# Performance work log

Hardware: AMD Instinct MI355X
Metric: run time of the kernel (lower is better)

Reference implementation:

```python
import jax, jax.numpy as jnp
import numpy as np

M = 8192      # nodes
D = 128       # feature dim
DEG = 32      # neighbors per node


def setup_inputs() -> dict:
    key = jax.random.key(0)
    ks = jax.random.split(key, 6)
    z = jax.random.normal(ks[0], (M, D), dtype=jnp.float32)
    # deterministic, duplicate-free edge list: node i -> (i+1..i+DEG) mod M
    src = jnp.repeat(jnp.arange(M, dtype=jnp.int64), DEG)
    dst = (src + jnp.tile(jnp.arange(1, DEG + 1, dtype=jnp.int64), M)) % M
    edge_index = jnp.stack([src, dst], axis=0)  # [2, M*DEG]
    s = 1.0 / np.sqrt(D)
    Wg = jax.random.normal(ks[1], (D, D), dtype=jnp.float32) * s
    Wc = jax.random.normal(ks[2], (D, D), dtype=jnp.float32) * s
    Wq = jax.random.normal(ks[3], (D, D), dtype=jnp.float32) * s
    Wk = jax.random.normal(ks[4], (D, D), dtype=jnp.float32) * s
    a = jax.random.normal(ks[5], (2 * D,), dtype=jnp.float32)
    return {"z": z, "edge_index": edge_index, "Wg": Wg, "Wc": Wc,
            "Wq": Wq, "Wk": Wk, "a": a}


def reference(z, edge_index, Wg, Wc, Wq, Wk, a):
    m, d = z.shape
    wg = z @ Wg.T                              # [m, d]
    src, dst = edge_index[0], edge_index[1]
    a_src, a_dst = a[:d], a[d:]
    # per-edge score: leaky_relu(a . [wg[i], wg[j]]) = leaky_relu(a1.wg[i] + a2.wg[j])
    scores = jax.nn.leaky_relu((wg @ a_src)[src] + (wg @ a_dst)[dst])  # [E]
    # softmax over each source node's neighbors (segment softmax)
    smax = jax.ops.segment_max(scores, src, num_segments=m)
    ex = jnp.exp(scores - smax[src])
    denom = jax.ops.segment_sum(ex, src, num_segments=m)
    alpha = ex / denom[src]                    # [E]
    # scatter-aggregate: local[i] = sum_j alpha_ij * wg[j]
    local = jax.ops.segment_sum(alpha[:, None] * wg[dst], src, num_segments=m)
    # dense global attention branch
    q = z @ Wq.T
    k = z @ Wk.T
    beta = jax.nn.softmax(q @ k.T / jnp.sqrt(jnp.float32(d)), axis=-1)  # [m, m]
    global_msg = beta @ (z @ Wc.T)
    return jax.nn.leaky_relu(local + global_msg + z)
```

## Files before the change

### kernel.cpp

```cpp
#include <hip/hip_runtime.h>

#define MM 8192
#define DD 128
#define DEG 32
#define KSPLIT 16
#define BK 32
#define NTILE 16
#define NB 16
#define RSTAGE 48

typedef __attribute__((ext_vector_type(8))) _Float16 h8;
typedef __attribute__((ext_vector_type(4))) float f4;
typedef __attribute__((ext_vector_type(4))) unsigned int u4;
typedef __attribute__((ext_vector_type(4))) short s4;

__device__ __forceinline__ unsigned short f2h(float f) {
  _Float16 h = (_Float16)f;
  return __builtin_bit_cast(unsigned short, h);
}

__device__ __forceinline__ void lds_dma16(const unsigned short* gptr, unsigned short* lptr) {
  __builtin_amdgcn_global_load_lds(
      (const __attribute__((address_space(1))) unsigned int*)gptr,
      (__attribute__((address_space(3))) unsigned int*)lptr, 16, 0, 0);
}

__global__ __launch_bounds__(256) void proj_kernel(
    const float* __restrict__ z, const float* __restrict__ Wg,
    const float* __restrict__ Wc, const float* __restrict__ Wq,
    const float* __restrict__ Wk, const float* __restrict__ a,
    float* __restrict__ wg, unsigned short* __restrict__ qb,
    unsigned short* __restrict__ kb, unsigned short* __restrict__ ct,
    float* __restrict__ sg, float* __restrict__ sd)
{
  __shared__ unsigned short zt[64 * 136];
  __shared__ unsigned short wt[128 * 136];
  const int mode = blockIdx.y;
  const float* __restrict__ W = (mode == 0) ? Wg : (mode == 1) ? Wq : (mode == 2) ? Wk : Wc;
  const int r0 = blockIdx.x * 64;
  const int tid = threadIdx.x;

  #pragma unroll
  for (int it = 0; it < 8; ++it) {
    int id = tid + it * 256, row = id >> 5, c4 = (id & 31) * 4;
    f4 v = *(const f4*)(z + (r0 + row) * DD + c4);
    s4 sv = {(short)f2h(v.x), (short)f2h(v.y), (short)f2h(v.z), (short)f2h(v.w)};
    *(s4*)&zt[row * 136 + c4] = sv;
  }
  #pragma unroll
  for (int it = 0; it < 16; ++it) {
    int id = tid + it * 256, row = id >> 5, c4 = (id & 31) * 4;
    f4 v = *(const f4*)(W + row * DD + c4);
    s4 sv = {(short)f2h(v.x), (short)f2h(v.y), (short)f2h(v.z), (short)f2h(v.w)};
    *(s4*)&wt[row * 136 + c4] = sv;
  }
  __syncthreads();

  const int lane = tid & 63, w = tid >> 6, n = lane & 15, quad = lane >> 4;
  h8 afr[4];
  #pragma unroll
  for (int kt = 0; kt < 4; ++kt)
    afr[kt] = *(const h8*)&zt[(16 * w + n) * 136 + kt * 32 + quad * 8];

  f4 acc[8];
  const f4 fzero = {0.f, 0.f, 0.f, 0.f};
  #pragma unroll
  for (int nt = 0; nt < 8; ++nt) {
    f4 c = fzero;
    #pragma unroll
    for (int kt = 0; kt < 4; ++kt) {
      h8 b = *(const h8*)&wt[(16 * nt + n) * 136 + kt * 32 + quad * 8];
      c = __builtin_amdgcn_mfma_f32_16x16x32_f16(afr[kt], b, c, 0, 0, 0);
    }
    acc[nt] = c;
  }

  if (mode == 0) {
    #pragma unroll
    for (int nt = 0; nt < 8; ++nt)
      #pragma unroll
      for (int r = 0; r < 4; ++r)
        wg[(r0 + 16 * w + quad * 4 + r) * DD + 16 * nt + n] = acc[nt][r];
    float av[8], bv[8];
    #pragma unroll
    for (int nt = 0; nt < 8; ++nt) { av[nt] = a[16 * nt + n]; bv[nt] = a[DD + 16 * nt + n]; }
    #pragma unroll
    for (int r = 0; r < 4; ++r) {
      float s1 = 0.f, s2 = 0.f;
      #pragma unroll
      for (int nt = 0; nt < 8; ++nt) { s1 += acc[nt][r] * av[nt]; s2 += acc[nt][r] * bv[nt]; }
      s1 += __shfl_xor(s1, 1); s1 += __shfl_xor(s1, 2); s1 += __shfl_xor(s1, 4); s1 += __shfl_xor(s1, 8);
      s2 += __shfl_xor(s2, 1); s2 += __shfl_xor(s2, 2); s2 += __shfl_xor(s2, 4); s2 += __shfl_xor(s2, 8);
      if (n == 0) {
        int g = r0 + 16 * w + quad * 4 + r;
        sg[g] = s1; sd[g] = s2;
      }
    }
  } else if (mode == 1) {
    const float qscale = 0.12752551286084110f;
    #pragma unroll
    for (int nt = 0; nt < 8; ++nt)
      #pragma unroll
      for (int r = 0; r < 4; ++r)
        qb[(r0 + 16 * w + quad * 4 + r) * DD + 16 * nt + n] = f2h(acc[nt][r] * qscale);
  } else if (mode == 2) {
    #pragma unroll
    for (int nt = 0; nt < 8; ++nt)
      #pragma unroll
      for (int r = 0; r < 4; ++r)
        kb[(r0 + 16 * w + quad * 4 + r) * DD + 16 * nt + n] = f2h(acc[nt][r]);
  } else {
    __syncthreads();
    #pragma unroll
    for (int nt = 0; nt < 8; ++nt)
      #pragma unroll
      for (int r = 0; r < 4; ++r)
        wt[(16 * nt + n) * 80 + 16 * w + quad * 4 + r] = f2h(acc[nt][r]);
    __syncthreads();
    #pragma unroll
    for (int it = 0; it < 4; ++it) {
      int idx = tid + it * 256, d = idx >> 3, c8 = (idx & 7) * 8;
      u4 v = *(const u4*)&wt[d * 80 + c8];
      *(u4*)(ct + (size_t)d * MM + r0 + c8) = v;
    }
  }
}

__global__ __launch_bounds__(256, 2) void flash_kernel(
    const unsigned short* __restrict__ qb, const unsigned short* __restrict__ kb,
    const unsigned short* __restrict__ ct, unsigned short* __restrict__ Opart,
    float* __restrict__ Lpart)
{
  __shared__ unsigned short sh[18944];
  const int bid = blockIdx.x + (blockIdx.y << 6);
  const int ck = bid & 15, qt = bid >> 4;
  const int tid = threadIdx.x, lane = tid & 63, w = tid >> 6;
  const int n = lane & 15, quad = lane >> 4;
  const int ln = n, lq = quad;
  const int qr0 = qt * 128;

  #pragma unroll
  for (int it = 0; it < 8; ++it)
    lds_dma16(qb + (qr0 + it * 16 + ln) * DD + w * 32 + lq * 8,
              &sh[(it * 256 + tid) * 8]);
  __syncthreads();
  h8 aq[2][4];
  #pragma unroll
  for (int mt = 0; mt < 2; ++mt)
    #pragma unroll
    for (int kt = 0; kt < 4; ++kt)
      aq[mt][kt] = *(const h8*)&sh[((w * 2 + mt) * 4 + kt) * 512 + lane * 8];
  __syncthreads();

  const unsigned short* kp = kb + (size_t)(ck * 512 + 2 * ln) * DD + w * 32 + lq * 8;
  const unsigned short* vp = ct + (size_t)(16 * w + ln) * MM + ck * 512 + lq * 8;

  #pragma unroll
  for (int it = 0; it < 2; ++it)
    lds_dma16(kp + it * DD, &sh[(it * 256 + tid) * 8]);
  #pragma unroll
  for (int it = 0; it < 2; ++it)
    lds_dma16(vp + (size_t)it * 64 * MM, &sh[4096 + (it * 256 + tid) * 8]);

  f4 acc_o[2][8];
  const f4 fzero = {0.f, 0.f, 0.f, 0.f};
  #pragma unroll
  for (int mt = 0; mt < 2; ++mt)
    #pragma unroll
    for (int dt = 0; dt < 8; ++dt) acc_o[mt][dt] = fzero;
  float l_r[2][4] = {{0.f, 0.f, 0.f, 0.f}, {0.f, 0.f, 0.f, 0.f}};
  const int pbase = 16384 + w * 640;

  for (int t = 0; t < NTILE; ++t) {
    __syncthreads();
    const int cur = (t & 1) * 8192;

    if (t < NTILE - 1) {
      const int nb = ((t + 1) & 1) * 8192;
      const unsigned short* kpn = kp + (size_t)(t + 1) * BK * DD;
      const unsigned short* vpn = vp + (t + 1) * BK;
      #pragma unroll
      for (int it = 0; it < 2; ++it)
        lds_dma16(kpn + it * DD, &sh[nb + (it * 256 + tid) * 8]);
      #pragma unroll
      for (int it = 0; it < 2; ++it)
        lds_dma16(vpn + (size_t)it * 64 * MM, &sh[nb + 4096 + (it * 256 + tid) * 8]);
    }

    f4 accs[2][2];
    accs[0][0] = fzero; accs[0][1] = fzero; accs[1][0] = fzero; accs[1][1] = fzero;
    __builtin_amdgcn_s_setprio(1);
    #pragma unroll
    for (int nt = 0; nt < 2; ++nt) {
      #pragma unroll
      for (int kt = 0; kt < 4; ++kt) {
        h8 bk = *(const h8*)&sh[cur + nt * 2048 + kt * 512 + lane * 8];
        accs[0][nt] = __builtin_amdgcn_mfma_f32_16x16x32_f16(aq[0][kt], bk, accs[0][nt], 0, 0, 0);
        accs[1][nt] = __builtin_amdgcn_mfma_f32_16x16x32_f16(aq[1][kt], bk, accs[1][nt], 0, 0, 0);
      }
    }
    __builtin_amdgcn_s_setprio(0);

    h8 ap[2];
    #pragma unroll
    for (int mt = 0; mt < 2; ++mt) {
      #pragma unroll
      for (int r = 0; r < 4; ++r) {
        float p0 = exp2f(fminf(accs[mt][0][r], 14.4269504f));
        float p1 = exp2f(fminf(accs[mt][1][r], 14.4269504f));
        l_r[mt][r] += p0 + p1;
        auto pv = __builtin_amdgcn_cvt_pkrtz(p0, p1);
        *(unsigned int*)&sh[pbase + (quad * 4 + r) * 40 + 2 * n] =
            __builtin_bit_cast(unsigned int, pv);
      }
      ap[mt] = *(const h8*)&sh[pbase + n * 40 + quad * 8];
    }

    __builtin_amdgcn_s_setprio(1);
    #pragma unroll
    for (int dt = 0; dt < 8; ++dt) {
      h8 bv = *(const h8*)&sh[cur + 4096 + dt * 512 + lane * 8];
      acc_o[0][dt] = __builtin_amdgcn_mfma_f32_16x16x32_f16(ap[0], bv, acc_o[0][dt], 0, 0, 0);
      acc_o[1][dt] = __builtin_amdgcn_mfma_f32_16x16x32_f16(ap[1], bv, acc_o[1][dt], 0, 0, 0);
    }
    __builtin_amdgcn_s_setprio(0);
  }

  #pragma unroll
  for (int mt = 0; mt < 2; ++mt)
    #pragma unroll
    for (int r = 0; r < 4; ++r) {
      float lv = l_r[mt][r];
      lv += __shfl_xor(lv, 1); lv += __shfl_xor(lv, 2);
      lv += __shfl_xor(lv, 4); lv += __shfl_xor(lv, 8);
      int g = qr0 + w * 32 + mt * 16 + quad * 4 + r;
      if (n == 0) Lpart[ck * MM + g] = lv;
      #pragma unroll
      for (int dt = 0; dt < 8; ++dt)
        Opart[((size_t)ck * MM + g) * DD + 16 * dt + n] = f2h(acc_o[mt][dt][r]);
    }
}

__global__ __launch_bounds__(256) void merge_kernel(
    const int* __restrict__ ei, const float* __restrict__ wg,
    const float* __restrict__ sg, const float* __restrict__ sd,
    const unsigned short* __restrict__ Opart, const float* __restrict__ Lpart,
    const float* __restrict__ z, float* __restrict__ out)
{
  __shared__ float rows_s[RSTAGE * 132];
  __shared__ float sc_s[NB][DEG];
  __shared__ float alpha_s[NB][DEG];
  __shared__ int idx_s[NB][DEG];
  const int tid = threadIdx.x;
  const int i0 = blockIdx.x * NB;

  #pragma unroll
  for (int it = 0; it < 6; ++it) {
    int idx = tid + it * 256;
    int r = idx >> 5, c4 = (idx & 31) * 4;
    int grow = (i0 + 1 + r) & (MM - 1);
    *(f4*)&rows_s[r * 132 + c4] = *(const f4*)(wg + (size_t)grow * DD + c4);
  }
  #pragma unroll
  for (int it = 0; it < 2; ++it) {
    int e = tid + it * 256;
    int nj = e >> 5, j = e & 31;
    int i = i0 + nj;
    int dstj = ei[MM * DEG + i * DEG + j];
    float s = sg[i] + sd[dstj];
    sc_s[nj][j] = s > 0.f ? s : 0.01f * s;
    idx_s[nj][j] = (dstj - (i0 + 1)) & (MM - 1);
  }
  __syncthreads();

  const int ni = tid >> 4, l16 = tid & 15;
  {
    float s0 = sc_s[ni][l16], s1 = sc_s[ni][l16 + 16];
    float mx = fmaxf(s0, s1);
    mx = fmaxf(mx, __shfl_xor(mx, 1)); mx = fmaxf(mx, __shfl_xor(mx, 2));
    mx = fmaxf(mx, __shfl_xor(mx, 4)); mx = fmaxf(mx, __shfl_xor(mx, 8));
    float p0 = __expf(s0 - mx), p1 = __expf(s1 - mx);
    float sum = p0 + p1;
    sum += __shfl_xor(sum, 1); sum += __shfl_xor(sum, 2);
    sum += __shfl_xor(sum, 4); sum += __shfl_xor(sum, 8);
    float inv = 1.f / sum;
    alpha_s[ni][l16] = p0 * inv;
    alpha_s[ni][l16 + 16] = p1 * inv;
  }

  const int d0 = l16 * 8;
  const int i = i0 + ni;
  float acc[8] = {0.f, 0.f, 0.f, 0.f, 0.f, 0.f, 0.f, 0.f};
  #pragma unroll 4
  for (int j = 0; j < DEG; ++j) {
    float al = alpha_s[ni][j];
    int r = idx_s[ni][j];
    if (r < RSTAGE) {
      const float* src = &rows_s[r * 132 + d0];
      #pragma unroll
      for (int q = 0; q < 8; ++q) acc[q] += al * src[q];
    } else {
      const float* src = wg + (size_t)((i0 + 1 + r) & (MM - 1)) * DD + d0;
      #pragma unroll
      for (int q = 0; q < 8; ++q) acc[q] += al * src[q];
    }
  }

  float l = 0.f;
  float o[8] = {0.f, 0.f, 0.f, 0.f, 0.f, 0.f, 0.f, 0.f};
  #pragma unroll
  for (int ck = 0; ck < KSPLIT; ++ck) {
    l += Lpart[ck * MM + i];
    h8 v = *(const h8*)(Opart + ((size_t)ck * MM + i) * DD + d0);
    #pragma unroll
    for (int q = 0; q < 8; ++q) o[q] += (float)v[q];
  }
  float inv = 1.0f / l;
  const float* zp = z + (size_t)i * DD + d0;
  float* op = out + (size_t)i * DD + d0;
  #pragma unroll
  for (int q = 0; q < 8; ++q) {
    float r = o[q] * inv + acc[q] + zp[q];
    op[q] = r > 0.f ? r : 0.01f * r;
  }
}

extern "C" void kernel_launch(void* const* d_in, const int* in_sizes, int n_in,
                              void* d_out, int out_size, void* d_ws, size_t ws_size,
                              hipStream_t stream) {
  const float* z  = (const float*)d_in[0];
  const int*   ei = (const int*)d_in[1];
  const float* Wg = (const float*)d_in[2];
  const float* Wc = (const float*)d_in[3];
  const float* Wq = (const float*)d_in[4];
  const float* Wk = (const float*)d_in[5];
  const float* a  = (const float*)d_in[6];
  float* out = (float*)d_out;
  char* ws = (char*)d_ws;

  float*          wg    = (float*)(ws + 0);
  unsigned short* qb    = (unsigned short*)(ws + (4 << 20));
  unsigned short* kb    = (unsigned short*)(ws + (6 << 20));
  unsigned short* ct    = (unsigned short*)(ws + (8 << 20));
  float*          sg    = (float*)(ws + (10 << 20));
  float*          sd    = (float*)(ws + (10 << 20) + (64 << 10));
  unsigned short* Opart = (unsigned short*)(ws + (11 << 20));
  float*          Lpart = (float*)(ws + (43 << 20));

  proj_kernel<<<dim3(128, 4), 256, 0, stream>>>(z, Wg, Wc, Wq, Wk, a, wg, qb, kb, ct, sg, sd);
  flash_kernel<<<dim3(64, KSPLIT), 256, 0, stream>>>(qb, kb, ct, Opart, Lpart);
  merge_kernel<<<512, 256, 0, stream>>>(ei, wg, sg, sd, Opart, Lpart, z, out);
}
```

Baseline: 133.9 us.

## Software-pipeline flash loop: overlap QK of tile t with PV of tile t-1

```diff
diff --git a/kernel.cpp b/kernel.cpp
--- a/kernel.cpp
+++ b/kernel.cpp
@@ -136,12 +136,11 @@
   const int ck = bid & 15, qt = bid >> 4;
   const int tid = threadIdx.x, lane = tid & 63, w = tid >> 6;
   const int n = lane & 15, quad = lane >> 4;
-  const int ln = n, lq = quad;
   const int qr0 = qt * 128;
 
   #pragma unroll
   for (int it = 0; it < 8; ++it)
-    lds_dma16(qb + (qr0 + it * 16 + ln) * DD + w * 32 + lq * 8,
+    lds_dma16(qb + (qr0 + it * 16 + n) * DD + w * 32 + quad * 8,
               &sh[(it * 256 + tid) * 8]);
   __syncthreads();
   h8 aq[2][4];
@@ -152,17 +151,16 @@
       aq[mt][kt] = *(const h8*)&sh[((w * 2 + mt) * 4 + kt) * 512 + lane * 8];
   __syncthreads();
 
-  const unsigned short* kp = kb + (size_t)(ck * 512 + 2 * ln) * DD + w * 32 + lq * 8;
-  const unsigned short* vp = ct + (size_t)(16 * w + ln) * MM + ck * 512 + lq * 8;
+  const unsigned short* kp = kb + (size_t)(ck * 512 + 2 * n) * DD + w * 32 + quad * 8;
+  const unsigned short* vp = ct + (size_t)(16 * w + n) * MM + ck * 512 + quad * 8;
 
   #pragma unroll
   for (int it = 0; it < 2; ++it)
     lds_dma16(kp + it * DD, &sh[(it * 256 + tid) * 8]);
-  #pragma unroll
-  for (int it = 0; it < 2; ++it)
-    lds_dma16(vp + (size_t)it * 64 * MM, &sh[4096 + (it * 256 + tid) * 8]);
 
   f4 acc_o[2][8];
+  f4 accs[2][2];
+  h8 ap[2];
   const f4 fzero = {0.f, 0.f, 0.f, 0.f};
   #pragma unroll
   for (int mt = 0; mt < 2; ++mt)
@@ -171,60 +169,82 @@
   float l_r[2][4] = {{0.f, 0.f, 0.f, 0.f}, {0.f, 0.f, 0.f, 0.f}};
   const int pbase = 16384 + w * 640;
 
-  for (int t = 0; t < NTILE; ++t) {
+#define QK_TILE(CUR)                                                          \
+  { accs[0][0] = fzero; accs[0][1] = fzero;                                   \
+    accs[1][0] = fzero; accs[1][1] = fzero;                                   \
+    __builtin_amdgcn_s_setprio(1);                                            \
+    _Pragma("unroll")                                                         \
+    for (int nt = 0; nt < 2; ++nt) {                                          \
+      _Pragma("unroll")                                                       \
+      for (int kt = 0; kt < 4; ++kt) {                                        \
+        h8 bk = *(const h8*)&sh[(CUR) + nt * 2048 + kt * 512 + lane * 8];     \
+        accs[0][nt] = __builtin_amdgcn_mfma_f32_16x16x32_f16(aq[0][kt], bk, accs[0][nt], 0, 0, 0); \
+        accs[1][nt] = __builtin_amdgcn_mfma_f32_16x16x32_f16(aq[1][kt], bk, accs[1][nt], 0, 0, 0); \
+      }                                                                       \
+    }                                                                         \
+    __builtin_amdgcn_s_setprio(0); }
+
+#define PV_TILE(PRV)                                                          \
+  { __builtin_amdgcn_s_setprio(1);                                            \
+    _Pragma("unroll")                                                         \
+    for (int dt = 0; dt < 8; ++dt) {                                          \
+      h8 bv = *(const h8*)&sh[(PRV) + 4096 + dt * 512 + lane * 8];            \
+      acc_o[0][dt] = __builtin_amdgcn_mfma_f32_16x16x32_f16(ap[0], bv, acc_o[0][dt], 0, 0, 0); \
+      acc_o[1][dt] = __builtin_amdgcn_mfma_f32_16x16x32_f16(ap[1], bv, acc_o[1][dt], 0, 0, 0); \
+    }                                                                         \
+    __builtin_amdgcn_s_setprio(0); }
+
+#define SOFTMAX_TILE                                                          \
+  { _Pragma("unroll")                                                         \
+    for (int mt = 0; mt < 2; ++mt) {                                          \
+      _Pragma("unroll")                                                       \
+      for (int r = 0; r < 4; ++r) {                                           \
+        float p0 = exp2f(fminf(accs[mt][0][r], 14.4269504f));                 \
+        float p1 = exp2f(fminf(accs[mt][1][r], 14.4269504f));                 \
+        l_r[mt][r] += p0 + p1;                                                \
+        auto pv2 = __builtin_amdgcn_cvt_pkrtz(p0, p1);      \
+        *(unsigned int*)&sh[pbase + (quad * 4 + r) * 40 + 2 * n] =            \
+            __builtin_bit_cast(unsigned int, pv2);                            \
+      }                                                                       \
+      ap[mt] = *(const h8*)&sh[pbase + n * 40 + quad * 8];                    \
+    }                                                                         \
+  }
+
+  __syncthreads();
+  #pragma unroll
+  for (int it = 0; it < 2; ++it)
+    lds_dma16(kp + BK * DD + it * DD, &sh[8192 + (it * 256 + tid) * 8]);
+  #pragma unroll
+  for (int it = 0; it < 2; ++it)
+    lds_dma16(vp + (size_t)it * 64 * MM, &sh[4096 + (it * 256 + tid) * 8]);
+  QK_TILE(0)
+  SOFTMAX_TILE
+
+  for (int t = 1; t < NTILE; ++t) {
     __syncthreads();
     const int cur = (t & 1) * 8192;
+    const int prv = cur ^ 8192;
 
     if (t < NTILE - 1) {
-      const int nb = ((t + 1) & 1) * 8192;
       const unsigned short* kpn = kp + (size_t)(t + 1) * BK * DD;
-      const unsigned short* vpn = vp + (t + 1) * BK;
       #pragma unroll
       for (int it = 0; it < 2; ++it)
-        lds_dma16(kpn + it * DD, &sh[nb + (it * 256 + tid) * 8]);
+        lds_dma16(kpn + it * DD, &sh[prv + (it * 256 + tid) * 8]);
+    }
+    {
+      const unsigned short* vpn = vp + t * BK;
       #pragma unroll
       for (int it = 0; it < 2; ++it)
-        lds_dma16(vpn + (size_t)it * 64 * MM, &sh[nb + 4096 + (it * 256 + tid) * 8]);
-    }
-
-    f4 accs[2][2];
-    accs[0][0] = fzero; accs[0][1] = fzero; accs[1][0] = fzero; accs[1][1] = fzero;
-    __builtin_amdgcn_s_setprio(1);
-    #pragma unroll
-    for (int nt = 0; nt < 2; ++nt) {
-      #pragma unroll
-      for (int kt = 0; kt < 4; ++kt) {
-        h8 bk = *(const h8*)&sh[cur + nt * 2048 + kt * 512 + lane * 8];
-        accs[0][nt] = __builtin_amdgcn_mfma_f32_16x16x32_f16(aq[0][kt], bk, accs[0][nt], 0, 0, 0);
-        accs[1][nt] = __builtin_amdgcn_mfma_f32_16x16x32_f16(aq[1][kt], bk, accs[1][nt], 0, 0, 0);
-      }
-    }
-    __builtin_amdgcn_s_setprio(0);
-
-    h8 ap[2];
-    #pragma unroll
-    for (int mt = 0; mt < 2; ++mt) {
-      #pragma unroll
-      for (int r = 0; r < 4; ++r) {
-        float p0 = exp2f(fminf(accs[mt][0][r], 14.4269504f));
-        float p1 = exp2f(fminf(accs[mt][1][r], 14.4269504f));
-        l_r[mt][r] += p0 + p1;
-        auto pv = __builtin_amdgcn_cvt_pkrtz(p0, p1);
-        *(unsigned int*)&sh[pbase + (quad * 4 + r) * 40 + 2 * n] =
-            __builtin_bit_cast(unsigned int, pv);
-      }
-      ap[mt] = *(const h8*)&sh[pbase + n * 40 + quad * 8];
-    }
-
-    __builtin_amdgcn_s_setprio(1);
-    #pragma unroll
-    for (int dt = 0; dt < 8; ++dt) {
-      h8 bv = *(const h8*)&sh[cur + 4096 + dt * 512 + lane * 8];
-      acc_o[0][dt] = __builtin_amdgcn_mfma_f32_16x16x32_f16(ap[0], bv, acc_o[0][dt], 0, 0, 0);
-      acc_o[1][dt] = __builtin_amdgcn_mfma_f32_16x16x32_f16(ap[1], bv, acc_o[1][dt], 0, 0, 0);
-    }
-    __builtin_amdgcn_s_setprio(0);
-  }
+        lds_dma16(vpn + (size_t)it * 64 * MM, &sh[cur + 4096 + (it * 256 + tid) * 8]);
+    }
+
+    QK_TILE(cur)
+    PV_TILE(prv)
+    SOFTMAX_TILE
+  }
+
+  __syncthreads();
+  PV_TILE(8192)
 
   #pragma unroll
   for (int mt = 0; mt < 2; ++mt)
@@ -239,6 +259,9 @@
       for (int dt = 0; dt < 8; ++dt)
         Opart[((size_t)ck * MM + g) * DD + 16 * dt + n] = f2h(acc_o[mt][dt][r]);
     }
+#undef QK_TILE
+#undef PV_TILE
+#undef SOFTMAX_TILE
 }
 
 __global__ __launch_bounds__(256) void merge_kernel(
```

Result: no change. 133.7 us (-0.1%).

## Halve flash KV splits, double key tile width, add nontemporal partial stores

Applied to the files above, without the earlier changes.

```diff
diff --git a/kernel.cpp b/kernel.cpp
--- a/kernel.cpp
+++ b/kernel.cpp
@@ -3,8 +3,8 @@
 #define MM 8192
 #define DD 128
 #define DEG 32
-#define KSPLIT 16
-#define BK 32
+#define KSPLIT 8
+#define BK 64
 #define NTILE 16
 #define NB 16
 #define RSTAGE 48
@@ -131,17 +131,16 @@
     const unsigned short* __restrict__ ct, unsigned short* __restrict__ Opart,
     float* __restrict__ Lpart)
 {
-  __shared__ unsigned short sh[18944];
+  __shared__ unsigned short sh[37376];
   const int bid = blockIdx.x + (blockIdx.y << 6);
-  const int ck = bid & 15, qt = bid >> 4;
+  const int ck = bid & 7, qt = bid >> 3;
   const int tid = threadIdx.x, lane = tid & 63, w = tid >> 6;
   const int n = lane & 15, quad = lane >> 4;
-  const int ln = n, lq = quad;
   const int qr0 = qt * 128;
 
   #pragma unroll
   for (int it = 0; it < 8; ++it)
-    lds_dma16(qb + (qr0 + it * 16 + ln) * DD + w * 32 + lq * 8,
+    lds_dma16(qb + (qr0 + it * 16 + n) * DD + w * 32 + quad * 8,
               &sh[(it * 256 + tid) * 8]);
   __syncthreads();
   h8 aq[2][4];
@@ -152,15 +151,15 @@
       aq[mt][kt] = *(const h8*)&sh[((w * 2 + mt) * 4 + kt) * 512 + lane * 8];
   __syncthreads();
 
-  const unsigned short* kp = kb + (size_t)(ck * 512 + 2 * ln) * DD + w * 32 + lq * 8;
-  const unsigned short* vp = ct + (size_t)(16 * w + ln) * MM + ck * 512 + lq * 8;
-
-  #pragma unroll
-  for (int it = 0; it < 2; ++it)
+  const unsigned short* kp = kb + (size_t)(ck * 1024 + 4 * n) * DD + w * 32 + quad * 8;
+  const unsigned short* vp = ct + (size_t)(16 * (w >> 1) + n) * MM + ck * 1024 + (w & 1) * 32 + quad * 8;
+
+  #pragma unroll
+  for (int it = 0; it < 4; ++it)
     lds_dma16(kp + it * DD, &sh[(it * 256 + tid) * 8]);
   #pragma unroll
-  for (int it = 0; it < 2; ++it)
-    lds_dma16(vp + (size_t)it * 64 * MM, &sh[4096 + (it * 256 + tid) * 8]);
+  for (int it = 0; it < 4; ++it)
+    lds_dma16(vp + (size_t)it * 32 * MM, &sh[8192 + (it * 256 + tid) * 8]);
 
   f4 acc_o[2][8];
   const f4 fzero = {0.f, 0.f, 0.f, 0.f};
@@ -169,29 +168,31 @@
     #pragma unroll
     for (int dt = 0; dt < 8; ++dt) acc_o[mt][dt] = fzero;
   float l_r[2][4] = {{0.f, 0.f, 0.f, 0.f}, {0.f, 0.f, 0.f, 0.f}};
-  const int pbase = 16384 + w * 640;
+  const int pbase = 32768 + w * 1152;
 
   for (int t = 0; t < NTILE; ++t) {
     __syncthreads();
-    const int cur = (t & 1) * 8192;
+    const int cur = (t & 1) * 16384;
 
     if (t < NTILE - 1) {
-      const int nb = ((t + 1) & 1) * 8192;
+      const int nb = ((t + 1) & 1) * 16384;
       const unsigned short* kpn = kp + (size_t)(t + 1) * BK * DD;
       const unsigned short* vpn = vp + (t + 1) * BK;
       #pragma unroll
-      for (int it = 0; it < 2; ++it)
+      for (int it = 0; it < 4; ++it)
         lds_dma16(kpn + it * DD, &sh[nb + (it * 256 + tid) * 8]);
       #pragma unroll
-      for (int it = 0; it < 2; ++it)
-        lds_dma16(vpn + (size_t)it * 64 * MM, &sh[nb + 4096 + (it * 256 + tid) * 8]);
-    }
-
-    f4 accs[2][2];
-    accs[0][0] = fzero; accs[0][1] = fzero; accs[1][0] = fzero; accs[1][1] = fzero;
-    __builtin_amdgcn_s_setprio(1);
-    #pragma unroll
-    for (int nt = 0; nt < 2; ++nt) {
+      for (int it = 0; it < 4; ++it)
+        lds_dma16(vpn + (size_t)it * 32 * MM, &sh[nb + 8192 + (it * 256 + tid) * 8]);
+    }
+
+    f4 accs[2][4];
+    #pragma unroll
+    for (int mt = 0; mt < 2; ++mt)
+      #pragma unroll
+      for (int nt = 0; nt < 4; ++nt) accs[mt][nt] = fzero;
+    #pragma unroll
+    for (int nt = 0; nt < 4; ++nt) {
       #pragma unroll
       for (int kt = 0; kt < 4; ++kt) {
         h8 bk = *(const h8*)&sh[cur + nt * 2048 + kt * 512 + lane * 8];
@@ -199,31 +200,36 @@
         accs[1][nt] = __builtin_amdgcn_mfma_f32_16x16x32_f16(aq[1][kt], bk, accs[1][nt], 0, 0, 0);
       }
     }
-    __builtin_amdgcn_s_setprio(0);
-
-    h8 ap[2];
+
+    h8 ap[2][2];
     #pragma unroll
     for (int mt = 0; mt < 2; ++mt) {
       #pragma unroll
       for (int r = 0; r < 4; ++r) {
         float p0 = exp2f(fminf(accs[mt][0][r], 14.4269504f));
         float p1 = exp2f(fminf(accs[mt][1][r], 14.4269504f));
-        l_r[mt][r] += p0 + p1;
-        auto pv = __builtin_amdgcn_cvt_pkrtz(p0, p1);
-        *(unsigned int*)&sh[pbase + (quad * 4 + r) * 40 + 2 * n] =
-            __builtin_bit_cast(unsigned int, pv);
+        float p2 = exp2f(fminf(accs[mt][2][r], 14.4269504f));
+        float p3 = exp2f(fminf(accs[mt][3][r], 14.4269504f));
+        l_r[mt][r] += (p0 + p1) + (p2 + p3);
+        auto pk0 = __builtin_amdgcn_cvt_pkrtz(p0, p1);
+        auto pk1 = __builtin_amdgcn_cvt_pkrtz(p2, p3);
+        uint2 pv2; pv2.x = __builtin_bit_cast(unsigned int, pk0);
+        pv2.y = __builtin_bit_cast(unsigned int, pk1);
+        *(uint2*)&sh[pbase + (quad * 4 + r) * 72 + n * 4] = pv2;
       }
-      ap[mt] = *(const h8*)&sh[pbase + n * 40 + quad * 8];
-    }
-
-    __builtin_amdgcn_s_setprio(1);
+      ap[mt][0] = *(const h8*)&sh[pbase + n * 72 + quad * 8];
+      ap[mt][1] = *(const h8*)&sh[pbase + n * 72 + 32 + quad * 8];
+    }
+
     #pragma unroll
     for (int dt = 0; dt < 8; ++dt) {
-      h8 bv = *(const h8*)&sh[cur + 4096 + dt * 512 + lane * 8];
-      acc_o[0][dt] = __builtin_amdgcn_mfma_f32_16x16x32_f16(ap[0], bv, acc_o[0][dt], 0, 0, 0);
-      acc_o[1][dt] = __builtin_amdgcn_mfma_f32_16x16x32_f16(ap[1], bv, acc_o[1][dt], 0, 0, 0);
-    }
-    __builtin_amdgcn_s_setprio(0);
+      #pragma unroll
+      for (int k2 = 0; k2 < 2; ++k2) {
+        h8 bv = *(const h8*)&sh[cur + 8192 + dt * 1024 + k2 * 512 + lane * 8];
+        acc_o[0][dt] = __builtin_amdgcn_mfma_f32_16x16x32_f16(ap[0][k2], bv, acc_o[0][dt], 0, 0, 0);
+        acc_o[1][dt] = __builtin_amdgcn_mfma_f32_16x16x32_f16(ap[1][k2], bv, acc_o[1][dt], 0, 0, 0);
+      }
+    }
   }
 
   #pragma unroll
@@ -234,10 +240,11 @@
       lv += __shfl_xor(lv, 1); lv += __shfl_xor(lv, 2);
       lv += __shfl_xor(lv, 4); lv += __shfl_xor(lv, 8);
       int g = qr0 + w * 32 + mt * 16 + quad * 4 + r;
-      if (n == 0) Lpart[ck * MM + g] = lv;
+      if (n == 0) __builtin_nontemporal_store(lv, &Lpart[ck * MM + g]);
       #pragma unroll
       for (int dt = 0; dt < 8; ++dt)
-        Opart[((size_t)ck * MM + g) * DD + 16 * dt + n] = f2h(acc_o[mt][dt][r]);
+        __builtin_nontemporal_store(f2h(acc_o[mt][dt][r]),
+                                    &Opart[((size_t)ck * MM + g) * DD + 16 * dt + n]);
     }
 }
 
@@ -310,8 +317,8 @@
   float o[8] = {0.f, 0.f, 0.f, 0.f, 0.f, 0.f, 0.f, 0.f};
   #pragma unroll
   for (int ck = 0; ck < KSPLIT; ++ck) {
-    l += Lpart[ck * MM + i];
-    h8 v = *(const h8*)(Opart + ((size_t)ck * MM + i) * DD + d0);
+    l += __builtin_nontemporal_load(&Lpart[ck * MM + i]);
+    h8 v = __builtin_nontemporal_load((const h8*)(Opart + ((size_t)ck * MM + i) * DD + d0));
     #pragma unroll
     for (int q = 0; q < 8; ++q) o[q] += (float)v[q];
   }
@@ -345,7 +352,7 @@
   float*          sg    = (float*)(ws + (10 << 20));
   float*          sd    = (float*)(ws + (10 << 20) + (64 << 10));
   unsigned short* Opart = (unsigned short*)(ws + (11 << 20));
-  float*          Lpart = (float*)(ws + (43 << 20));
+  float*          Lpart = (float*)(ws + (27 << 20));
 
   proj_kernel<<<dim3(128, 4), 256, 0, stream>>>(z, Wg, Wc, Wq, Wk, a, wg, qb, kb, ct, sg, sd);
   flash_kernel<<<dim3(64, KSPLIT), 256, 0, stream>>>(qb, kb, ct, Opart, Lpart);
```

Result: no change. 133.4 us (-0.4%).
